# Kernel optimization log

Measured on AMD Instinct MI355X. Metric: run time of the kernel, lower is better.

The kernel has to match this reference:

```python
import jax, jax.numpy as jnp
import numpy as np

ALPHA = 0.2        # LeakyReLU slope inside attention layers
OUT_SLOPE = 0.01   # F.leaky_relu default slope on the final output
EPS = 1e-16        # guards isolated nodes (pyGAT divides by rowsum directly)


def _sp_layer(x, src, dst, W, a, concat, n_nodes):
    # x: [N, F_in], W: [F_in, F_out], a: [2*F_out]
    h = x @ W                                            # [N, F_out]
    eh = jnp.concatenate([h[src], h[dst]], axis=1)       # [E, 2*F_out]
    e = jnp.exp(-jax.nn.leaky_relu(eh @ a, ALPHA))       # [E] unnormalized attn
    denom = jax.ops.segment_sum(e, src, num_segments=n_nodes)          # [N]
    agg = jax.ops.segment_sum(e[:, None] * h[dst], src, num_segments=n_nodes)  # [N, F_out]
    hp = agg / (denom[:, None] + EPS)
    return jax.nn.elu(hp) if concat else hp


def _forward_one(xb, eib, W_heads, a_heads, W_out, a_out):
    n = xb.shape[0]
    src, dst = eib[0], eib[1]
    # independent heads (static small loop), concat on feature dim
    heads = [_sp_layer(xb, src, dst, W_heads[h], a_heads[h], True, n)
             for h in range(W_heads.shape[0])]
    xc = jnp.concatenate(heads, axis=1)                  # [N, nheads*nhid]
    out = _sp_layer(xc, src, dst, W_out, a_out, False, n)  # [N, nclass]
    return jax.nn.leaky_relu(out, OUT_SLOPE)


def setup_inputs() -> dict:
    key = jax.random.key(0)
    B, N, E = 8, 10000, 160000
    nfeat, nhid, nclass, nheads = 256, 64, 64, 8
    ks = jax.random.split(key, 6)
    x = jax.random.normal(ks[0], (B, N, nfeat), dtype=jnp.float32)
    edge_index = jax.random.randint(ks[1], (B, 2, E), 0, N, dtype=jnp.int32)
    # xavier-normal-ish init scales
    W_heads = jax.random.normal(ks[2], (nheads, nfeat, nhid), dtype=jnp.float32) * np.sqrt(2.0 / (nfeat + nhid))
    a_heads = jax.random.normal(ks[3], (nheads, 2 * nhid), dtype=jnp.float32) * np.sqrt(2.0 / (2 * nhid + 1))
    W_out = jax.random.normal(ks[4], (nheads * nhid, nclass), dtype=jnp.float32) * np.sqrt(2.0 / (nheads * nhid + nclass))
    a_out = jax.random.normal(ks[5], (2 * nclass,), dtype=jnp.float32) * np.sqrt(2.0 / (2 * nclass + 1))
    return {"x": x, "edge_index": edge_index, "W_heads": W_heads,
            "a_heads": a_heads, "W_out": W_out, "a_out": a_out, "batch_size": B}


def reference(x, edge_index, W_heads, a_heads, W_out, a_out, batch_size):
    # batch loop in the original is a pure map over graphs -> vmap
    return jax.vmap(lambda xb, eib: _forward_one(xb, eib, W_heads, a_heads, W_out, a_out))(x, edge_index)
```

## Files before the change

### kernel.cpp

```cpp
#include <hip/hip_runtime.h>
#include <cstdint>
#include <cstddef>

#define NND   10000
#define NED   160000
#define NB    8
#define NF    256
#define NHID  64
#define HEADS 8
#define F1    512
#define NCLS  64

#define NSH   8
#define NBUCK 40
#define CHUNK 4096

#define ALPHA_SLOPE 0.2f
#define OUT_SLOPE   0.01f
#define EPS         1e-16f

typedef unsigned short u16;
typedef short short8 __attribute__((ext_vector_type(8)));
typedef float f32x4 __attribute__((ext_vector_type(4)));

static const size_t B_WCHI = 0;
static const size_t B_WCLO = 262144;
static const size_t B_WOHI = 524288;
static const size_t B_WOLO = 589824;
static const size_t B_AS1  = 655360;
static const size_t B_AD1  = 3215360;
static const size_t B_AS2  = 5775360;
static const size_t B_AD2  = 6095360;
static const size_t B_CNT  = 6415360;
static const size_t B_BCUR = 6735360;
static const size_t B_ROWS = 6739456;
static const size_t B_TMP  = 7059520;
static const size_t B_DST  = 12179520;
static const size_t B_SCR  = 14739520;
#define ZSTRU 16000000ull
static const size_t S_PERZ = 2 * ZSTRU;

__device__ __forceinline__ u16 f32_to_bf16_rn(float f) {
  uint32_t u = __float_as_uint(f);
  uint32_t r = u + 0x7fffu + ((u >> 16) & 1u);
  return (u16)(r >> 16);
}
__device__ __forceinline__ float bf16_to_f32(u16 s) {
  return __uint_as_float((uint32_t)s << 16);
}
__device__ __forceinline__ void split1(float v, u16& h, u16& l) {
  h = f32_to_bf16_rn(v);
  float r = v - bf16_to_f32(h);
  l = f32_to_bf16_rn(r);
}

__global__ __launch_bounds__(256) void k_wsplit1(const float* __restrict__ Whd,
                                                 u16* __restrict__ hi,
                                                 u16* __restrict__ lo) {
  int t = blockIdx.x * 256 + threadIdx.x;
  int lane = t & 63;
  int frag = t >> 6;
  int nj = frag & 3;
  int w  = (frag >> 2) & 3;
  int ts = (frag >> 4) & 7;
  int by = frag >> 7;
  int lm = lane & 15, lkg = lane >> 4;
  int n = by * 256 + w * 64 + nj * 16 + lm;
  int h = n >> 6, nc = n & 63;
  u16 hv[8], lv[8];
#pragma unroll
  for (int j = 0; j < 8; ++j) {
    int k = ts * 32 + lkg * 8 + j;
    split1(Whd[h * (NF * NHID) + k * NHID + nc], hv[j], lv[j]);
  }
  size_t o = (size_t)t * 8;
  *(ushort4*)(hi + o) = make_ushort4(hv[0], hv[1], hv[2], hv[3]);
  *(ushort4*)(hi + o + 4) = make_ushort4(hv[4], hv[5], hv[6], hv[7]);
  *(ushort4*)(lo + o) = make_ushort4(lv[0], lv[1], lv[2], lv[3]);
  *(ushort4*)(lo + o + 4) = make_ushort4(lv[4], lv[5], lv[6], lv[7]);
}
__global__ __launch_bounds__(256) void k_wsplit2(const float* __restrict__ Wo,
                                                 u16* __restrict__ hi,
                                                 u16* __restrict__ lo) {
  int idx = blockIdx.x * 256 + threadIdx.x;
  int n = idx >> 9, k = idx & 511;
  float v = Wo[k * NCLS + n];
  u16 h, l; split1(v, h, l);
  hi[idx] = h; lo[idx] = l;
}

__global__ __launch_bounds__(256) void k_gemm1(
    const float* __restrict__ x,
    const u16* __restrict__ Bfh, const u16* __restrict__ Bfl,
    u16* __restrict__ h1_s,
    const float* __restrict__ avec,
    float* __restrict__ as_g, float* __restrict__ ad_g,
    int base_b, int zsh) {
  __shared__ u16 As_hi[64][40];
  __shared__ u16 As_lo[64][40];

  const int zmask = (1 << zsh) - 1;
  const int z = blockIdx.x & zmask;
  const int wg = blockIdx.x >> zsh;
  const int b = base_b + z;
  const float* A = x + (size_t)b * NND * NF;
  u16* C = h1_s + (size_t)z * ZSTRU;
  float* as_ = as_g + (size_t)b * NND * 8;
  float* ad_ = ad_g + (size_t)b * NND * 8;

  const int m0 = (wg >> 1) * 64;
  const int by = wg & 1;

  const int tid = threadIdx.x;
  const int lane = tid & 63;
  const int w = tid >> 6;
  const int lm = lane & 15;
  const int lkg = lane >> 4;
  const int hb = by * 4 + w;

  f32x4 acc[4][4];
#pragma unroll
  for (int mi = 0; mi < 4; ++mi)
#pragma unroll
    for (int nj = 0; nj < 4; ++nj) acc[mi][nj] = 0.f;

  for (int t = 0; t < 8; ++t) {
    const int kk = t * 32;
    __syncthreads();
#pragma unroll
    for (int u = 0; u < 2; ++u) {
      int e = u * 256 + tid;
      int rr = e >> 3, kf = (e & 7) * 4;
      int gm = m0 + rr;
      float4 v = make_float4(0.f, 0.f, 0.f, 0.f);
      if (gm < NND) v = *(const float4*)(A + (size_t)gm * NF + kk + kf);
      ushort4 hv, lv;
      split1(v.x, hv.x, lv.x); split1(v.y, hv.y, lv.y);
      split1(v.z, hv.z, lv.z); split1(v.w, hv.w, lv.w);
      *(ushort4*)&As_hi[rr][kf] = hv;
      *(ushort4*)&As_lo[rr][kf] = lv;
    }
    short8 bh[4], bl[4];
    {
      size_t fb = (((size_t)(by * 8 + t) * 4 + w) * 4) * 512 + (size_t)lane * 8;
#pragma unroll
      for (int nj = 0; nj < 4; ++nj) {
        bh[nj] = *(const short8*)(Bfh + fb + nj * 512);
        bl[nj] = *(const short8*)(Bfl + fb + nj * 512);
      }
    }
    __syncthreads();

    short8 ah[4], al[4];
#pragma unroll
    for (int mi = 0; mi < 4; ++mi) {
      int row = mi * 16 + lm;
      ah[mi] = *(const short8*)&As_hi[row][lkg * 8];
      al[mi] = *(const short8*)&As_lo[row][lkg * 8];
    }
#pragma unroll
    for (int mi = 0; mi < 4; ++mi)
#pragma unroll
      for (int nj = 0; nj < 4; ++nj) {
        acc[mi][nj] = __builtin_amdgcn_mfma_f32_16x16x32_bf16(ah[mi], bh[nj], acc[mi][nj], 0, 0, 0);
        acc[mi][nj] = __builtin_amdgcn_mfma_f32_16x16x32_bf16(ah[mi], bl[nj], acc[mi][nj], 0, 0, 0);
        acc[mi][nj] = __builtin_amdgcn_mfma_f32_16x16x32_bf16(al[mi], bh[nj], acc[mi][nj], 0, 0, 0);
      }
  }

  float a_sv[4], a_dv[4];
#pragma unroll
  for (int nj = 0; nj < 4; ++nj) {
    a_sv[nj] = avec[hb * 128 + nj * 16 + lm];
    a_dv[nj] = avec[hb * 128 + 64 + nj * 16 + lm];
  }
  const int n0 = by * 256 + w * 64;
#pragma unroll
  for (int mi = 0; mi < 4; ++mi) {
#pragma unroll
    for (int rr = 0; rr < 4; ++rr) {
      int gm = m0 + mi * 16 + lkg * 4 + rr;
      float ps = acc[mi][0][rr] * a_sv[0] + acc[mi][1][rr] * a_sv[1] +
                 acc[mi][2][rr] * a_sv[2] + acc[mi][3][rr] * a_sv[3];
      float pd = acc[mi][0][rr] * a_dv[0] + acc[mi][1][rr] * a_dv[1] +
                 acc[mi][2][rr] * a_dv[2] + acc[mi][3][rr] * a_dv[3];
#pragma unroll
      for (int off = 1; off < 16; off <<= 1) {
        ps += __shfl_xor(ps, off, 16);
        pd += __shfl_xor(pd, off, 16);
      }
      if (gm < NND) {
#pragma unroll
        for (int nj = 0; nj < 4; ++nj)
          C[(size_t)gm * F1 + n0 + nj * 16 + lm] = f32_to_bf16_rn(acc[mi][nj][rr]);
        if (lm == 0) {
          as_[(size_t)gm * 8 + hb] = ps;
          ad_[(size_t)gm * 8 + hb] = pd;
        }
      }
    }
  }
}

__global__ __launch_bounds__(256) void k_gemm2(
    const u16* __restrict__ Ahi_s, const u16* __restrict__ Alo_s,
    const u16* __restrict__ Bhi, const u16* __restrict__ Blo,
    u16* __restrict__ C_s,
    const float* __restrict__ avec,
    float* __restrict__ as_g, float* __restrict__ ad_g,
    int base_b, int zsh) {
  __shared__ u16 As_hi[64][40];
  __shared__ u16 As_lo[64][40];
  __shared__ u16 Bs_hi[64][40];
  __shared__ u16 Bs_lo[64][40];

  const int zmask = (1 << zsh) - 1;
  const int z = blockIdx.x & zmask;
  const int wg = blockIdx.x >> zsh;
  const int b = base_b + z;
  const u16* Ahi = Ahi_s + (size_t)z * ZSTRU;
  const u16* Alo = Alo_s + (size_t)z * ZSTRU;
  u16* C = C_s + (size_t)z * ZSTRU;
  float* as_ = as_g + (size_t)b * NND;
  float* ad_ = ad_g + (size_t)b * NND;

  const int tid = threadIdx.x;
  const int lane = tid & 63;
  const int w = tid >> 6;
  const int lm = lane & 15;
  const int lkg = lane >> 4;
  const int m0 = wg * 64;

  f32x4 acc[4];
#pragma unroll
  for (int j = 0; j < 4; ++j) acc[j] = 0.f;

  for (int kk = 0; kk < F1; kk += 32) {
    __syncthreads();
#pragma unroll
    for (int u = 0; u < 2; ++u) {
      int e = u * 256 + tid;
      int rr = e >> 3, kf = (e & 7) * 4;
      int gm = m0 + rr;
      ushort4 hv = make_ushort4(0, 0, 0, 0), lv = make_ushort4(0, 0, 0, 0);
      if (gm < NND) {
        size_t g = (size_t)gm * F1 + kk + kf;
        hv = *(const ushort4*)(Ahi + g);
        lv = *(const ushort4*)(Alo + g);
      }
      *(ushort4*)&As_hi[rr][kf] = hv;
      *(ushort4*)&As_lo[rr][kf] = lv;
    }
#pragma unroll
    for (int u = 0; u < 2; ++u) {
      int e = u * 256 + tid;
      int n = e >> 3, kf = (e & 7) * 4;
      size_t g = (size_t)n * F1 + kk + kf;
      *(ushort4*)&Bs_hi[n][kf] = *(const ushort4*)(Bhi + g);
      *(ushort4*)&Bs_lo[n][kf] = *(const ushort4*)(Blo + g);
    }
    __syncthreads();

    short8 ah, al, bh[4], bl[4];
    {
      int row = w * 16 + lm;
      ah = *(const short8*)&As_hi[row][lkg * 8];
      al = *(const short8*)&As_lo[row][lkg * 8];
    }
#pragma unroll
    for (int nj = 0; nj < 4; ++nj) {
      int row = nj * 16 + lm;
      bh[nj] = *(const short8*)&Bs_hi[row][lkg * 8];
      bl[nj] = *(const short8*)&Bs_lo[row][lkg * 8];
    }
#pragma unroll
    for (int nj = 0; nj < 4; ++nj) {
      acc[nj] = __builtin_amdgcn_mfma_f32_16x16x32_bf16(ah, bh[nj], acc[nj], 0, 0, 0);
      acc[nj] = __builtin_amdgcn_mfma_f32_16x16x32_bf16(ah, bl[nj], acc[nj], 0, 0, 0);
      acc[nj] = __builtin_amdgcn_mfma_f32_16x16x32_bf16(al, bh[nj], acc[nj], 0, 0, 0);
    }
  }

  float a_sv[4], a_dv[4];
#pragma unroll
  for (int nj = 0; nj < 4; ++nj) {
    a_sv[nj] = avec[nj * 16 + lm];
    a_dv[nj] = avec[64 + nj * 16 + lm];
  }
#pragma unroll
  for (int rr = 0; rr < 4; ++rr) {
    int gm = m0 + w * 16 + lkg * 4 + rr;
    float ps = acc[0][rr] * a_sv[0] + acc[1][rr] * a_sv[1] +
               acc[2][rr] * a_sv[2] + acc[3][rr] * a_sv[3];
    float pd = acc[0][rr] * a_dv[0] + acc[1][rr] * a_dv[1] +
               acc[2][rr] * a_dv[2] + acc[3][rr] * a_dv[3];
#pragma unroll
    for (int off = 1; off < 16; off <<= 1) {
      ps += __shfl_xor(ps, off, 16);
      pd += __shfl_xor(pd, off, 16);
    }
    if (gm < NND) {
#pragma unroll
      for (int nj = 0; nj < 4; ++nj)
        C[(size_t)gm * NCLS + nj * 16 + lm] = f32_to_bf16_rn(acc[nj][rr]);
      if (lm == 0) {
        as_[gm] = ps;
        ad_[gm] = pd;
      }
    }
  }
}


__global__ __launch_bounds__(256) void k_hist(const int* __restrict__ ei,
                                              int* __restrict__ counts) {
  int b = blockIdx.y;
  int e4 = (blockIdx.x * 256 + threadIdx.x) * 4;
  if (e4 < NED) {
    int4 s = *(const int4*)(ei + (size_t)b * 2 * NED + e4);
    atomicAdd(&counts[b * NND + s.x], 1);
    atomicAdd(&counts[b * NND + s.y], 1);
    atomicAdd(&counts[b * NND + s.z], 1);
    atomicAdd(&counts[b * NND + s.w], 1);
  }
}

__global__ __launch_bounds__(1024) void k_scan(const int* __restrict__ counts,
                                               int* __restrict__ rows) {
  __shared__ int lds[1024];
  const int b = blockIdx.x;
  const int tid = threadIdx.x;
  const int* cb = counts + b * NND;
  int* rb = rows + b * (NND + 1);
  int v[10];
  int s = 0;
  int base = tid * 10;
#pragma unroll
  for (int j = 0; j < 10; ++j) {
    int i = base + j;
    v[j] = (i < NND) ? cb[i] : 0;
    s += v[j];
  }
  lds[tid] = s;
  __syncthreads();
  for (int off = 1; off < 1024; off <<= 1) {
    int t = (tid >= off) ? lds[tid - off] : 0;
    __syncthreads();
    lds[tid] += t;
    __syncthreads();
  }
  int run = lds[tid] - s;
#pragma unroll
  for (int j = 0; j < 10; ++j) {
    int i = base + j;
    if (i < NND) rb[i] = run;
    run += v[j];
  }
  if (tid == 1023) rb[NND] = run;
}

__global__ __launch_bounds__(256) void k_scat_a(const int* __restrict__ ei,
                                                const int* __restrict__ rows,
                                                int* __restrict__ bcur,
                                                unsigned* __restrict__ tmp) {
  __shared__ unsigned stage[CHUNK];
  __shared__ int cnt[NBUCK], off[NBUCK], cur[NBUCK], gb[NBUCK];
  const int b = blockIdx.y;
  const int e0 = blockIdx.x * CHUNK;
  const int nE = min(CHUNK, NED - e0);
  const int tid = threadIdx.x;
  const int* sb = ei + (size_t)b * 2 * NED;
  const int* db = sb + NED;

  for (int k = tid; k < NBUCK; k += 256) cnt[k] = 0;
  __syncthreads();
  for (int j = tid; j < nE; j += 256)
    atomicAdd(&cnt[sb[e0 + j] >> NSH], 1);
  __syncthreads();
  if (tid == 0) {
    int run = 0;
    for (int k = 0; k < NBUCK; ++k) { off[k] = run; run += cnt[k]; }
  }
  __syncthreads();
  for (int k = tid; k < NBUCK; k += 256) cur[k] = off[k];
  __syncthreads();
  for (int j = tid; j < nE; j += 256) {
    int s = sb[e0 + j], d = db[e0 + j];
    int p = atomicAdd(&cur[s >> NSH], 1);
    stage[p] = ((unsigned)s << 16) | (unsigned)d;
  }
  __syncthreads();
  for (int k = tid; k < NBUCK; k += 256) {
    int c = cnt[k];
    gb[k] = c ? rows[b * (NND + 1) + (k << NSH)] + atomicAdd(&bcur[b * NBUCK + k], c)
              : 0;
  }
  __syncthreads();
  for (int i = tid; i < nE; i += 256) {
    unsigned p = stage[i];
    int k = (int)(p >> 16) >> NSH;
    tmp[(size_t)b * NED + gb[k] + (i - off[k])] = p;
  }
}

__global__ __launch_bounds__(256) void k_scat_b(const int* __restrict__ rows,
                                                const unsigned* __restrict__ tmp,
                                                u16* __restrict__ dst_s) {
  __shared__ int cur[256];
  const int k = blockIdx.x, b = blockIdx.y;
  const int* rb = rows + b * (NND + 1);
  const int n0 = k << NSH;
  const int tid = threadIdx.x;
  cur[tid] = rb[min(n0 + tid, NND)];
  __syncthreads();
  const int beg = rb[n0];
  const int end = rb[min(n0 + 256, NND)];
  for (int i = beg + tid; i < end; i += 256) {
    unsigned p = tmp[(size_t)b * NED + i];
    int pos = atomicAdd(&cur[(int)(p >> 16) - n0], 1);
    dst_s[(size_t)b * NED + pos] = (u16)(p & 0xffffu);
  }
}

#define UPK8(q, e) do { \
  acc[0] = fmaf(e, __uint_as_float((q).x << 16), acc[0]); \
  acc[1] = fmaf(e, __uint_as_float((q).x & 0xffff0000u), acc[1]); \
  acc[2] = fmaf(e, __uint_as_float((q).y << 16), acc[2]); \
  acc[3] = fmaf(e, __uint_as_float((q).y & 0xffff0000u), acc[3]); \
  acc[4] = fmaf(e, __uint_as_float((q).z << 16), acc[4]); \
  acc[5] = fmaf(e, __uint_as_float((q).z & 0xffff0000u), acc[5]); \
  acc[6] = fmaf(e, __uint_as_float((q).w << 16), acc[6]); \
  acc[7] = fmaf(e, __uint_as_float((q).w & 0xffff0000u), acc[7]); \
} while (0)

#define LKY(t) ((t) >= 0.f ? (t) : ALPHA_SLOPE * (t))

__global__ __launch_bounds__(256) void k_agg1(
    const int* __restrict__ rows_g, const u16* __restrict__ dst_g,
    const u16* __restrict__ h1_s,
    const float* __restrict__ as_g, const float* __restrict__ ad_g,
    u16* __restrict__ xchi_s, u16* __restrict__ xclo_s,
    int base_b, int zsh) {
  const int zmask = (1 << zsh) - 1;
  const int z = blockIdx.x & zmask;
  const int idx = blockIdx.x >> zsh;
  const int b = base_b + z;
  const int* rows = rows_g + (size_t)b * (NND + 1);
  const u16* dst = dst_g + (size_t)b * NED;
  const u16* h1 = h1_s + (size_t)z * ZSTRU;
  const float* as_ = as_g + (size_t)b * NND * 8;
  const float* ad_ = ad_g + (size_t)b * NND * 8;
  u16* xh = xchi_s + (size_t)z * ZSTRU;
  u16* xl = xclo_s + (size_t)z * ZSTRU;

  int lane = threadIdx.x & 63;
  int n = (idx * 256 + threadIdx.x) >> 6;
  if (n >= NND) return;
  const int hh = lane >> 3;
  const float asv = as_[n * 8 + hh];
  int beg = rows[n], end = rows[n + 1];
  float acc[8] = {};
  float den = 0.f;
  int i = beg;
  for (; i + 4 <= end; i += 4) {
    int d0 = dst[i], d1 = dst[i + 1], d2 = dst[i + 2], d3 = dst[i + 3];
    float t0 = LKY(asv + ad_[d0 * 8 + hh]);
    float t1 = LKY(asv + ad_[d1 * 8 + hh]);
    float t2 = LKY(asv + ad_[d2 * 8 + hh]);
    float t3 = LKY(asv + ad_[d3 * 8 + hh]);
    float e0 = __expf(-t0), e1 = __expf(-t1);
    float e2 = __expf(-t2), e3 = __expf(-t3);
    uint4 q0 = *((const uint4*)(h1 + (size_t)d0 * F1) + lane);
    uint4 q1 = *((const uint4*)(h1 + (size_t)d1 * F1) + lane);
    uint4 q2 = *((const uint4*)(h1 + (size_t)d2 * F1) + lane);
    uint4 q3 = *((const uint4*)(h1 + (size_t)d3 * F1) + lane);
    UPK8(q0, e0); UPK8(q1, e1); UPK8(q2, e2); UPK8(q3, e3);
    den += (e0 + e1) + (e2 + e3);
  }
  for (; i < end; ++i) {
    int d0 = dst[i];
    float t0 = LKY(asv + ad_[d0 * 8 + hh]);
    float e0 = __expf(-t0);
    uint4 q0 = *((const uint4*)(h1 + (size_t)d0 * F1) + lane);
    UPK8(q0, e0);
    den += e0;
  }
  float inv = 1.f / (den + EPS);
  u16 oh[8], ol[8];
#pragma unroll
  for (int j = 0; j < 8; ++j) {
    float v = acc[j] * inv;
    v = v > 0.f ? v : expm1f(v);
    split1(v, oh[j], ol[j]);
  }
  size_t wo = (size_t)n * F1 + lane * 8;
  *(ushort4*)(xh + wo) = make_ushort4(oh[0], oh[1], oh[2], oh[3]);
  *(ushort4*)(xh + wo + 4) = make_ushort4(oh[4], oh[5], oh[6], oh[7]);
  *(ushort4*)(xl + wo) = make_ushort4(ol[0], ol[1], ol[2], ol[3]);
  *(ushort4*)(xl + wo + 4) = make_ushort4(ol[4], ol[5], ol[6], ol[7]);
}

__global__ __launch_bounds__(256) void k_agg2(
    const int* __restrict__ rows_g, const u16* __restrict__ dst_g,
    const u16* __restrict__ h2_s,
    const float* __restrict__ as_g, const float* __restrict__ ad_g,
    float* __restrict__ out, int base_b, int zsh) {
  const int zmask = (1 << zsh) - 1;
  const int z = blockIdx.x & zmask;
  const int idx = blockIdx.x >> zsh;
  const int b = base_b + z;
  const int* rows = rows_g + (size_t)b * (NND + 1);
  const u16* dst = dst_g + (size_t)b * NED;
  const u16* h2 = h2_s + (size_t)z * ZSTRU;
  const float* as_ = as_g + (size_t)b * NND;
  const float* ad_ = ad_g + (size_t)b * NND;
  float* ob = out + (size_t)b * NND * NCLS;

  int lane = threadIdx.x & 63;
  int n = (idx * 256 + threadIdx.x) >> 6;
  if (n >= NND) return;
  const float asv = as_[n];
  int beg = rows[n], end = rows[n + 1];
  float acc = 0.f, den = 0.f;
  int i = beg;
  for (; i + 4 <= end; i += 4) {
    int d0 = dst[i], d1 = dst[i + 1], d2 = dst[i + 2], d3 = dst[i + 3];
    float t0 = LKY(asv + ad_[d0]);
    float t1 = LKY(asv + ad_[d1]);
    float t2 = LKY(asv + ad_[d2]);
    float t3 = LKY(asv + ad_[d3]);
    float e0 = __expf(-t0), e1 = __expf(-t1);
    float e2 = __expf(-t2), e3 = __expf(-t3);
    float h0 = bf16_to_f32(h2[(size_t)d0 * NCLS + lane]);
    float h1v = bf16_to_f32(h2[(size_t)d1 * NCLS + lane]);
    float h2v = bf16_to_f32(h2[(size_t)d2 * NCLS + lane]);
    float h3v = bf16_to_f32(h2[(size_t)d3 * NCLS + lane]);
    acc = fmaf(e0, h0, acc); acc = fmaf(e1, h1v, acc);
    acc = fmaf(e2, h2v, acc); acc = fmaf(e3, h3v, acc);
    den += (e0 + e1) + (e2 + e3);
  }
  for (; i < end; ++i) {
    int d0 = dst[i];
    float t0 = LKY(asv + ad_[d0]);
    float e0 = __expf(-t0);
    acc = fmaf(e0, bf16_to_f32(h2[(size_t)d0 * NCLS + lane]), acc);
    den += e0;
  }
  float v = acc / (den + EPS);
  ob[(size_t)n * NCLS + lane] = v >= 0.f ? v : OUT_SLOPE * v;
}

extern "C" void kernel_launch(void* const* d_in, const int* in_sizes, int n_in,
                              void* d_out, int out_size, void* d_ws, size_t ws_size,
                              hipStream_t stream) {
  const float* x       = (const float*)d_in[0];
  const int*   ei      = (const int*)d_in[1];
  const float* W_heads = (const float*)d_in[2];
  const float* a_heads = (const float*)d_in[3];
  const float* W_out   = (const float*)d_in[4];
  const float* a_out   = (const float*)d_in[5];
  float* out = (float*)d_out;

  char* base = (char*)d_ws;
  u16* wchi = (u16*)(base + B_WCHI);
  u16* wclo = (u16*)(base + B_WCLO);
  u16* wohi = (u16*)(base + B_WOHI);
  u16* wolo = (u16*)(base + B_WOLO);
  float* as1 = (float*)(base + B_AS1);
  float* ad1 = (float*)(base + B_AD1);
  float* as2 = (float*)(base + B_AS2);
  float* ad2 = (float*)(base + B_AD2);
  int* counts    = (int*)(base + B_CNT);
  int* bcur      = (int*)(base + B_BCUR);
  int* rows      = (int*)(base + B_ROWS);
  unsigned* tmp  = (unsigned*)(base + B_TMP);
  u16* dst_s     = (u16*)(base + B_DST);
  u16* scr       = (u16*)(base + B_SCR);

  int Z = 1, zsh = 0;
  if (ws_size >= B_SCR + 8 * S_PERZ) { Z = 8; zsh = 3; }
  else if (ws_size >= B_SCR + 4 * S_PERZ) { Z = 4; zsh = 2; }
  else if (ws_size >= B_SCR + 2 * S_PERZ) { Z = 2; zsh = 1; }

  u16* xchi = scr + 0;
  u16* xclo = scr + 5120000;
  u16* h1   = scr + 10240000;
  u16* h2   = scr + 15360000;

  k_wsplit1<<<64, 256, 0, stream>>>(W_heads, wchi, wclo);
  k_wsplit2<<<(NCLS * F1) / 256, 256, 0, stream>>>(W_out, wohi, wolo);

  hipMemsetAsync(counts, 0, B_ROWS - B_CNT, stream);
  k_hist<<<dim3((NED / 4 + 255) / 256, NB), 256, 0, stream>>>(ei, counts);
  k_scan<<<NB, 1024, 0, stream>>>(counts, rows);
  k_scat_a<<<dim3((NED + CHUNK - 1) / CHUNK, NB), 256, 0, stream>>>(ei, rows, bcur, tmp);
  k_scat_b<<<dim3(NBUCK, NB), 256, 0, stream>>>(rows, tmp, dst_s);

  const int nwg1 = ((NND + 63) / 64) * 2;
  const int nwg2 = (NND + 63) / 64;
  for (int bb = 0; bb < NB; bb += Z) {
    k_gemm1<<<dim3(nwg1 << zsh), 256, 0, stream>>>(
        x, wchi, wclo, h1, a_heads, as1, ad1, bb, zsh);
    k_agg1<<<dim3(2500 << zsh), 256, 0, stream>>>(rows, dst_s, h1, as1, ad1,
                                                  xchi, xclo, bb, zsh);
    k_gemm2<<<dim3(nwg2 << zsh), 256, 0, stream>>>(
        xchi, xclo, wohi, wolo, h2, a_out, as2, ad2, bb, zsh);
    k_agg2<<<dim3(2500 << zsh), 256, 0, stream>>>(rows, dst_s, h2, as2, ad2,
                                                  out, bb, zsh);
  }
  (void)in_sizes; (void)n_in; (void)out_size;
}
```

Baseline: 454.0 us.

## Simplify CSR build, widen gemm1 blocks, and preload gemm2 B fragments

Three separate changes. The two-pass bucketed scatter is replaced by a single atomic-cursor scatter, with the cursor initialised in the scan kernel. gemm1 moves to 512-thread blocks that cover all 512 output columns per 64-row tile, so each x tile is loaded and split once instead of twice. gemm2 drops its LDS staging of B and reads pre-swizzled MFMA fragments straight from global memory, like gemm1. The new scatter leaves edge order within a row nondeterministic and may cost more global atomics.

```diff
diff --git a/kernel.cpp b/kernel.cpp
--- a/kernel.cpp
+++ b/kernel.cpp
@@ -10,10 +10,6 @@
 #define HEADS 8
 #define F1    512
 #define NCLS  64
-
-#define NSH   8
-#define NBUCK 40
-#define CHUNK 4096
 
 #define ALPHA_SLOPE 0.2f
 #define OUT_SLOPE   0.01f
@@ -61,11 +57,11 @@
   int lane = t & 63;
   int frag = t >> 6;
   int nj = frag & 3;
-  int w  = (frag >> 2) & 3;
+  int wq = (frag >> 2) & 3;
   int ts = (frag >> 4) & 7;
   int by = frag >> 7;
   int lm = lane & 15, lkg = lane >> 4;
-  int n = by * 256 + w * 64 + nj * 16 + lm;
+  int n = by * 256 + wq * 64 + nj * 16 + lm;
   int h = n >> 6, nc = n & 63;
   u16 hv[8], lv[8];
 #pragma unroll
@@ -79,17 +75,30 @@
   *(ushort4*)(lo + o) = make_ushort4(lv[0], lv[1], lv[2], lv[3]);
   *(ushort4*)(lo + o + 4) = make_ushort4(lv[4], lv[5], lv[6], lv[7]);
 }
+
 __global__ __launch_bounds__(256) void k_wsplit2(const float* __restrict__ Wo,
                                                  u16* __restrict__ hi,
                                                  u16* __restrict__ lo) {
-  int idx = blockIdx.x * 256 + threadIdx.x;
-  int n = idx >> 9, k = idx & 511;
-  float v = Wo[k * NCLS + n];
-  u16 h, l; split1(v, h, l);
-  hi[idx] = h; lo[idx] = l;
-}
-
-__global__ __launch_bounds__(256) void k_gemm1(
+  int t = blockIdx.x * 256 + threadIdx.x;
+  int lane = t & 63;
+  int frag = t >> 6;
+  int nj = frag & 3, ts = frag >> 2;
+  int lm = lane & 15, lkg = lane >> 4;
+  int n = nj * 16 + lm;
+  u16 hv[8], lv[8];
+#pragma unroll
+  for (int j = 0; j < 8; ++j) {
+    int k = ts * 32 + lkg * 8 + j;
+    split1(Wo[k * NCLS + n], hv[j], lv[j]);
+  }
+  size_t o = (size_t)t * 8;
+  *(ushort4*)(hi + o) = make_ushort4(hv[0], hv[1], hv[2], hv[3]);
+  *(ushort4*)(hi + o + 4) = make_ushort4(hv[4], hv[5], hv[6], hv[7]);
+  *(ushort4*)(lo + o) = make_ushort4(lv[0], lv[1], lv[2], lv[3]);
+  *(ushort4*)(lo + o + 4) = make_ushort4(lv[4], lv[5], lv[6], lv[7]);
+}
+
+__global__ __launch_bounds__(512) void k_gemm1(
     const float* __restrict__ x,
     const u16* __restrict__ Bfh, const u16* __restrict__ Bfl,
     u16* __restrict__ h1_s,
@@ -108,15 +117,13 @@
   float* as_ = as_g + (size_t)b * NND * 8;
   float* ad_ = ad_g + (size_t)b * NND * 8;
 
-  const int m0 = (wg >> 1) * 64;
-  const int by = wg & 1;
-
+  const int m0 = wg * 64;
   const int tid = threadIdx.x;
   const int lane = tid & 63;
   const int w = tid >> 6;
   const int lm = lane & 15;
   const int lkg = lane >> 4;
-  const int hb = by * 4 + w;
+  const int by = w >> 2, wq = w & 3;
 
   f32x4 acc[4][4];
 #pragma unroll
@@ -127,10 +134,8 @@
   for (int t = 0; t < 8; ++t) {
     const int kk = t * 32;
     __syncthreads();
-#pragma unroll
-    for (int u = 0; u < 2; ++u) {
-      int e = u * 256 + tid;
-      int rr = e >> 3, kf = (e & 7) * 4;
+    {
+      int rr = tid >> 3, kf = (tid & 7) * 4;
       int gm = m0 + rr;
       float4 v = make_float4(0.f, 0.f, 0.f, 0.f);
       if (gm < NND) v = *(const float4*)(A + (size_t)gm * NF + kk + kf);
@@ -142,7 +147,7 @@
     }
     short8 bh[4], bl[4];
     {
-      size_t fb = (((size_t)(by * 8 + t) * 4 + w) * 4) * 512 + (size_t)lane * 8;
+      size_t fb = (((size_t)(by * 8 + t) * 4 + wq) * 4) * 512 + (size_t)lane * 8;
 #pragma unroll
       for (int nj = 0; nj < 4; ++nj) {
         bh[nj] = *(const short8*)(Bfh + fb + nj * 512);
@@ -168,13 +173,14 @@
       }
   }
 
+  const int hb = w;
+  const int n0 = w * 64;
   float a_sv[4], a_dv[4];
 #pragma unroll
   for (int nj = 0; nj < 4; ++nj) {
     a_sv[nj] = avec[hb * 128 + nj * 16 + lm];
     a_dv[nj] = avec[hb * 128 + 64 + nj * 16 + lm];
   }
-  const int n0 = by * 256 + w * 64;
 #pragma unroll
   for (int mi = 0; mi < 4; ++mi) {
 #pragma unroll
@@ -204,15 +210,13 @@
 
 __global__ __launch_bounds__(256) void k_gemm2(
     const u16* __restrict__ Ahi_s, const u16* __restrict__ Alo_s,
-    const u16* __restrict__ Bhi, const u16* __restrict__ Blo,
+    const u16* __restrict__ Bfh, const u16* __restrict__ Bfl,
     u16* __restrict__ C_s,
     const float* __restrict__ avec,
     float* __restrict__ as_g, float* __restrict__ ad_g,
     int base_b, int zsh) {
   __shared__ u16 As_hi[64][40];
   __shared__ u16 As_lo[64][40];
-  __shared__ u16 Bs_hi[64][40];
-  __shared__ u16 Bs_lo[64][40];
 
   const int zmask = (1 << zsh) - 1;
   const int z = blockIdx.x & zmask;
@@ -235,7 +239,8 @@
 #pragma unroll
   for (int j = 0; j < 4; ++j) acc[j] = 0.f;
 
-  for (int kk = 0; kk < F1; kk += 32) {
+  for (int ts = 0; ts < 16; ++ts) {
+    const int kk = ts * 32;
     __syncthreads();
 #pragma unroll
     for (int u = 0; u < 2; ++u) {
@@ -251,27 +256,22 @@
       *(ushort4*)&As_hi[rr][kf] = hv;
       *(ushort4*)&As_lo[rr][kf] = lv;
     }
-#pragma unroll
-    for (int u = 0; u < 2; ++u) {
-      int e = u * 256 + tid;
-      int n = e >> 3, kf = (e & 7) * 4;
-      size_t g = (size_t)n * F1 + kk + kf;
-      *(ushort4*)&Bs_hi[n][kf] = *(const ushort4*)(Bhi + g);
-      *(ushort4*)&Bs_lo[n][kf] = *(const ushort4*)(Blo + g);
+    short8 bh[4], bl[4];
+    {
+      size_t fb = (size_t)(ts * 4) * 512 + (size_t)lane * 8;
+#pragma unroll
+      for (int nj = 0; nj < 4; ++nj) {
+        bh[nj] = *(const short8*)(Bfh + fb + nj * 512);
+        bl[nj] = *(const short8*)(Bfl + fb + nj * 512);
+      }
     }
     __syncthreads();
 
-    short8 ah, al, bh[4], bl[4];
+    short8 ah, al;
     {
       int row = w * 16 + lm;
       ah = *(const short8*)&As_hi[row][lkg * 8];
       al = *(const short8*)&As_lo[row][lkg * 8];
-    }
-#pragma unroll
-    for (int nj = 0; nj < 4; ++nj) {
-      int row = nj * 16 + lm;
-      bh[nj] = *(const short8*)&Bs_hi[row][lkg * 8];
-      bl[nj] = *(const short8*)&Bs_lo[row][lkg * 8];
     }
 #pragma unroll
     for (int nj = 0; nj < 4; ++nj) {
@@ -314,24 +314,27 @@
 
 __global__ __launch_bounds__(256) void k_hist(const int* __restrict__ ei,
                                               int* __restrict__ counts) {
-  int b = blockIdx.y;
-  int e4 = (blockIdx.x * 256 + threadIdx.x) * 4;
+  int z = blockIdx.x & 7;
+  int blk = blockIdx.x >> 3;
+  int e4 = (blk * 256 + threadIdx.x) * 4;
   if (e4 < NED) {
-    int4 s = *(const int4*)(ei + (size_t)b * 2 * NED + e4);
-    atomicAdd(&counts[b * NND + s.x], 1);
-    atomicAdd(&counts[b * NND + s.y], 1);
-    atomicAdd(&counts[b * NND + s.z], 1);
-    atomicAdd(&counts[b * NND + s.w], 1);
+    int4 s = *(const int4*)(ei + (size_t)z * 2 * NED + e4);
+    atomicAdd(&counts[z * NND + s.x], 1);
+    atomicAdd(&counts[z * NND + s.y], 1);
+    atomicAdd(&counts[z * NND + s.z], 1);
+    atomicAdd(&counts[z * NND + s.w], 1);
   }
 }
 
 __global__ __launch_bounds__(1024) void k_scan(const int* __restrict__ counts,
-                                               int* __restrict__ rows) {
+                                               int* __restrict__ rows,
+                                               int* __restrict__ cursor) {
   __shared__ int lds[1024];
   const int b = blockIdx.x;
   const int tid = threadIdx.x;
   const int* cb = counts + b * NND;
   int* rb = rows + b * (NND + 1);
+  int* ub = cursor + b * NND;
   int v[10];
   int s = 0;
   int base = tid * 10;
@@ -353,72 +356,23 @@
 #pragma unroll
   for (int j = 0; j < 10; ++j) {
     int i = base + j;
-    if (i < NND) rb[i] = run;
+    if (i < NND) { rb[i] = run; ub[i] = run; }
     run += v[j];
   }
   if (tid == 1023) rb[NND] = run;
 }
 
-__global__ __launch_bounds__(256) void k_scat_a(const int* __restrict__ ei,
-                                                const int* __restrict__ rows,
-                                                int* __restrict__ bcur,
-                                                unsigned* __restrict__ tmp) {
-  __shared__ unsigned stage[CHUNK];
-  __shared__ int cnt[NBUCK], off[NBUCK], cur[NBUCK], gb[NBUCK];
-  const int b = blockIdx.y;
-  const int e0 = blockIdx.x * CHUNK;
-  const int nE = min(CHUNK, NED - e0);
-  const int tid = threadIdx.x;
-  const int* sb = ei + (size_t)b * 2 * NED;
-  const int* db = sb + NED;
-
-  for (int k = tid; k < NBUCK; k += 256) cnt[k] = 0;
-  __syncthreads();
-  for (int j = tid; j < nE; j += 256)
-    atomicAdd(&cnt[sb[e0 + j] >> NSH], 1);
-  __syncthreads();
-  if (tid == 0) {
-    int run = 0;
-    for (int k = 0; k < NBUCK; ++k) { off[k] = run; run += cnt[k]; }
-  }
-  __syncthreads();
-  for (int k = tid; k < NBUCK; k += 256) cur[k] = off[k];
-  __syncthreads();
-  for (int j = tid; j < nE; j += 256) {
-    int s = sb[e0 + j], d = db[e0 + j];
-    int p = atomicAdd(&cur[s >> NSH], 1);
-    stage[p] = ((unsigned)s << 16) | (unsigned)d;
-  }
-  __syncthreads();
-  for (int k = tid; k < NBUCK; k += 256) {
-    int c = cnt[k];
-    gb[k] = c ? rows[b * (NND + 1) + (k << NSH)] + atomicAdd(&bcur[b * NBUCK + k], c)
-              : 0;
-  }
-  __syncthreads();
-  for (int i = tid; i < nE; i += 256) {
-    unsigned p = stage[i];
-    int k = (int)(p >> 16) >> NSH;
-    tmp[(size_t)b * NED + gb[k] + (i - off[k])] = p;
-  }
-}
-
-__global__ __launch_bounds__(256) void k_scat_b(const int* __restrict__ rows,
-                                                const unsigned* __restrict__ tmp,
-                                                u16* __restrict__ dst_s) {
-  __shared__ int cur[256];
-  const int k = blockIdx.x, b = blockIdx.y;
-  const int* rb = rows + b * (NND + 1);
-  const int n0 = k << NSH;
-  const int tid = threadIdx.x;
-  cur[tid] = rb[min(n0 + tid, NND)];
-  __syncthreads();
-  const int beg = rb[n0];
-  const int end = rb[min(n0 + 256, NND)];
-  for (int i = beg + tid; i < end; i += 256) {
-    unsigned p = tmp[(size_t)b * NED + i];
-    int pos = atomicAdd(&cur[(int)(p >> 16) - n0], 1);
-    dst_s[(size_t)b * NED + pos] = (u16)(p & 0xffffu);
+__global__ __launch_bounds__(256) void k_scatter(const int* __restrict__ ei,
+                                                 int* __restrict__ cursor,
+                                                 u16* __restrict__ dst_s) {
+  int z = blockIdx.x & 7;
+  int blk = blockIdx.x >> 3;
+  int e = blk * 256 + threadIdx.x;
+  if (e < NED) {
+    int s = ei[(size_t)z * 2 * NED + e];
+    int d = ei[(size_t)z * 2 * NED + NED + e];
+    int pos = atomicAdd(&cursor[z * NND + s], 1);
+    dst_s[(size_t)z * NED + pos] = (u16)d;
   }
 }
 
@@ -571,9 +525,8 @@
   float* as2 = (float*)(base + B_AS2);
   float* ad2 = (float*)(base + B_AD2);
   int* counts    = (int*)(base + B_CNT);
-  int* bcur      = (int*)(base + B_BCUR);
   int* rows      = (int*)(base + B_ROWS);
-  unsigned* tmp  = (unsigned*)(base + B_TMP);
+  int* cursor    = (int*)(base + B_TMP);
   u16* dst_s     = (u16*)(base + B_DST);
   u16* scr       = (u16*)(base + B_SCR);
 
@@ -588,22 +541,20 @@
   u16* h2   = scr + 15360000;
 
   k_wsplit1<<<64, 256, 0, stream>>>(W_heads, wchi, wclo);
-  k_wsplit2<<<(NCLS * F1) / 256, 256, 0, stream>>>(W_out, wohi, wolo);
-
-  hipMemsetAsync(counts, 0, B_ROWS - B_CNT, stream);
-  k_hist<<<dim3((NED / 4 + 255) / 256, NB), 256, 0, stream>>>(ei, counts);
-  k_scan<<<NB, 1024, 0, stream>>>(counts, rows);
-  k_scat_a<<<dim3((NED + CHUNK - 1) / CHUNK, NB), 256, 0, stream>>>(ei, rows, bcur, tmp);
-  k_scat_b<<<dim3(NBUCK, NB), 256, 0, stream>>>(rows, tmp, dst_s);
-
-  const int nwg1 = ((NND + 63) / 64) * 2;
-  const int nwg2 = (NND + 63) / 64;
+  k_wsplit2<<<16, 256, 0, stream>>>(W_out, wohi, wolo);
+
+  hipMemsetAsync(counts, 0, (size_t)NB * NND * sizeof(int), stream);
+  k_hist<<<dim3(((NED / 4 + 255) / 256) * 8), 256, 0, stream>>>(ei, counts);
+  k_scan<<<NB, 1024, 0, stream>>>(counts, rows, cursor);
+  k_scatter<<<dim3(((NED + 255) / 256) * 8), 256, 0, stream>>>(ei, cursor, dst_s);
+
+  const int nwg = (NND + 63) / 64;
   for (int bb = 0; bb < NB; bb += Z) {
-    k_gemm1<<<dim3(nwg1 << zsh), 256, 0, stream>>>(
+    k_gemm1<<<dim3(nwg << zsh), 512, 0, stream>>>(
         x, wchi, wclo, h1, a_heads, as1, ad1, bb, zsh);
     k_agg1<<<dim3(2500 << zsh), 256, 0, stream>>>(rows, dst_s, h1, as1, ad1,
                                                   xchi, xclo, bb, zsh);
-    k_gemm2<<<dim3(nwg2 << zsh), 256, 0, stream>>>(
+    k_gemm2<<<dim3(nwg << zsh), 256, 0, stream>>>(
         xchi, xclo, wohi, wolo, h2, a_out, as2, ad2, bb, zsh);
     k_agg2<<<dim3(2500 << zsh), 256, 0, stream>>>(rows, dst_s, h2, as2, ad2,
                                                   out, bb, zsh);
```

Result: no change. 455.0 us (+0.2%).
